# Performance work log

Measured on AMD Instinct MI355X. Metric: run time of the kernel, lower is better.

The kernel has to match this reference:

```python
import jax, jax.numpy as jnp
import numpy as np

B, T, I, H = 64, 512, 256, 1024


def setup_inputs() -> dict:
    key = jax.random.key(0)
    ks = jax.random.split(key, 20)
    stdv = float(1.0 / np.sqrt(H))
    u = lambda k, shape: jax.random.uniform(k, shape, jnp.float32, -stdv, stdv)
    d = {
        "inputs": jax.random.normal(ks[0], (B, T, I), jnp.float32),
        "h0": jax.random.normal(ks[1], (1, B, H), jnp.float32),
        "c0": jax.random.normal(ks[2], (1, B, H), jnp.float32),
    }
    names = ["w_ii", "w_hi", "b_ii", "b_hi",
             "w_if", "w_hf", "b_if", "b_hf",
             "w_io", "w_ho", "b_io", "b_ho",
             "w_ig", "w_hg", "b_ig", "b_hg"]
    shapes = {"w_i": (H, I), "w_h": (H, H), "b_i": (H,), "b_h": (H,)}
    for j, n in enumerate(names):
        d[n] = u(ks[3 + j], shapes[n[:3]])
    return d


def reference(inputs, h0, c0,
              w_ii, w_hi, b_ii, b_hi,
              w_if, w_hf, b_if, b_hf,
              w_io, w_ho, b_io, b_ho,
              w_ig, w_hg, b_ig, b_hg):
    # Fuse the 4 gate GEMMs into one: gate order i, f, g, o.
    Wx = jnp.concatenate([w_ii, w_if, w_ig, w_io], axis=0)  # (4H, I)
    Wh = jnp.concatenate([w_hi, w_hf, w_hg, w_ho], axis=0)  # (4H, H)
    b = jnp.concatenate([b_ii + b_hi, b_if + b_hf, b_ig + b_hg, b_io + b_ho], axis=0)  # (4H,)
    # Precompute all input projections in one big GEMM: (T, B, 4H)
    x_proj = jnp.einsum('bti,gi->tbg', inputs, Wx) + b

    def step(carry, xp):
        h, c = carry                       # (B, H), (B, H)
        z = xp + h @ Wh.T                  # (B, 4H)
        i = jax.nn.sigmoid(z[:, :H])
        f = jax.nn.sigmoid(z[:, H:2 * H])
        g = jnp.tanh(z[:, 2 * H:3 * H])
        o = jax.nn.sigmoid(z[:, 3 * H:])
        c = f * c + i * g
        h = o * jnp.tanh(c)
        return (h, c), h

    (h, c), hs = jax.lax.scan(step, (h0[0], c0[0]), x_proj)
    hidden_seq = jnp.transpose(hs, (1, 0, 2))  # (B, T, H)
    return hidden_seq, (h[None], c[None])
```

## Files before the change

kernel.cpp:

```cpp
#include <hip/hip_runtime.h>
#include <hip/hip_bf16.h>

#define TT 512
#define BB 64
#define II 256
#define HH 1024
#define NWG 256
#define MB 16
#define NJ 16
#define NR 64
#define KTOT 1280
#define WU 120
#define WROWB 1920
#define HROWB 2048
#define NFLAG 1024

typedef __bf16 bf16x8 __attribute__((ext_vector_type(8)));
typedef float f32x4 __attribute__((ext_vector_type(4)));
typedef unsigned uint32x4 __attribute__((ext_vector_type(4)));
typedef unsigned uint32x2 __attribute__((ext_vector_type(2)));

__device__ inline uint32x4 ld16_sc1(const void* p) {
  uint32x4 r;
  asm volatile("global_load_dwordx4 %0, %1, off sc1" : "=&v"(r) : "v"(p));
  return r;
}


__global__ __launch_bounds__(256) void k_cast_inputs(const float* __restrict__ in,
                                                     __hip_bfloat16* __restrict__ outp) {
  int i = (blockIdx.x * 256 + threadIdx.x) * 4;
  float4 v = *reinterpret_cast<const float4*>(in + i);
  outp[i + 0] = __float2bfloat16(v.x);
  outp[i + 1] = __float2bfloat16(v.y);
  outp[i + 2] = __float2bfloat16(v.z);
  outp[i + 3] = __float2bfloat16(v.w);
}

__global__ __launch_bounds__(256) void k_pack_w(
    const float* __restrict__ wxi, const float* __restrict__ whi,
    const float* __restrict__ wxf, const float* __restrict__ whf,
    const float* __restrict__ wxg, const float* __restrict__ whg,
    const float* __restrict__ wxo, const float* __restrict__ who,
    __hip_bfloat16* __restrict__ Wp) {
  int t = blockIdx.x * 256 + threadIdx.x;
  int p = t / 320;
  int k4 = (t - p * 320) * 4;
  int j = p >> 2, gate = p & 3;
  const float* wx = (gate == 0) ? wxi : (gate == 1) ? wxf : (gate == 2) ? wxg : wxo;
  const float* wh = (gate == 0) ? whi : (gate == 1) ? whf : (gate == 2) ? whg : who;
  float4 v;
  if (k4 < II) v = *reinterpret_cast<const float4*>(wx + (size_t)j * II + k4);
  else         v = *reinterpret_cast<const float4*>(wh + (size_t)j * HH + (k4 - II));
  __hip_bfloat16* o = Wp + (size_t)p * KTOT + k4;
  o[0] = __float2bfloat16(v.x);
  o[1] = __float2bfloat16(v.y);
  o[2] = __float2bfloat16(v.z);
  o[3] = __float2bfloat16(v.w);
}

__global__ __launch_bounds__(256) void k_pack_bias_h0(
    const float* __restrict__ bii, const float* __restrict__ bhi,
    const float* __restrict__ bif, const float* __restrict__ bhf,
    const float* __restrict__ bg,  const float* __restrict__ bhg,
    const float* __restrict__ bio, const float* __restrict__ bho,
    const float* __restrict__ h0, float* __restrict__ biasp,
    __hip_bfloat16* __restrict__ hb, unsigned* __restrict__ flags) {
  int i = blockIdx.x * 256 + threadIdx.x;
  if (i < 4096) {
    int j = i >> 2, gate = i & 3;
    const float* bi = (gate == 0) ? bii : (gate == 1) ? bif : (gate == 2) ? bg : bio;
    const float* bh = (gate == 0) ? bhi : (gate == 1) ? bhf : (gate == 2) ? bhg : bho;
    biasp[i] = bi[j] + bh[j];
  }
  if (i < NFLAG) flags[i] = 0;
  hb[i] = __float2bfloat16(h0[i]);
}


__global__ __launch_bounds__(256, 1) void k_lstm(
    const __hip_bfloat16* __restrict__ xb,
    const __hip_bfloat16* __restrict__ Wp,
    const float* __restrict__ biasp,
    const float* __restrict__ c0,
    __hip_bfloat16* __restrict__ hbuf,
    unsigned* __restrict__ flags,
    float* __restrict__ out)
{
  extern __shared__ __align__(16) char smem[];
  char* Wl = smem;
  char* Hs = smem + 122880;
  char* Zx = smem + 155648;
  char* Ho = smem + 160768;

  const int tid = threadIdx.x;
  const int lane = tid & 63;
  const int wq = tid >> 6;
  const int bt = blockIdx.x >> 6;
  const int gt = blockIdx.x & 63;
  const int b0 = bt * MB;
  const int r0 = gt * NR;

  const int l15 = lane & 15;
  const int kqu = lane >> 4;

  {
    const int u = tid & 127;
    const bool act = u < WU;
    uint32x4 tmp[16];
#pragma unroll
    for (int q = 0; q < 16; ++q) {
      int row = q * 2 + (tid >> 7);
      if (act) tmp[q] = *reinterpret_cast<const uint32x4*>(
          Wp + (size_t)(r0 + row) * KTOT + II + u * 8);
    }
#pragma unroll
    for (int q = 0; q < 16; ++q) {
      int row = q * 2 + (tid >> 7);
      if (act) *reinterpret_cast<uint32x4*>(Wl + row * WROWB + ((u ^ (row & 7)) << 4)) = tmp[q];
    }
#pragma unroll
    for (int q = 0; q < 16; ++q) {
      int row = 32 + q * 2 + (tid >> 7);
      if (act) tmp[q] = *reinterpret_cast<const uint32x4*>(
          Wp + (size_t)(r0 + row) * KTOT + II + u * 8);
    }
#pragma unroll
    for (int q = 0; q < 16; ++q) {
      int row = 32 + q * 2 + (tid >> 7);
      if (act) *reinterpret_cast<uint32x4*>(Wl + row * WROWB + ((u ^ (row & 7)) << 4)) = tmp[q];
    }
  }

  const int brow = r0 + wq * 16 + l15;
  bf16x8 wxr[8], wht0, wht1;
  {
    const __hip_bfloat16* ws = Wp + (size_t)brow * KTOT + kqu * 8;
#pragma unroll
    for (int kk = 0; kk < 8; ++kk)
      wxr[kk] = *reinterpret_cast<const bf16x8*>(ws + kk * 32);
    wht0 = *reinterpret_cast<const bf16x8*>(ws + II + 960);
    wht1 = *reinterpret_cast<const bf16x8*>(ws + II + 992);
  }

  const int m_e = 4 * kqu + (lane & 3);
  const int tq = (lane >> 2) & 3;
  const int j_g = gt * NJ + wq * 4 + tq;
  const int b_g = b0 + m_e;
  const float4 bias = *reinterpret_cast<const float4*>(biasp + j_g * 4);
  float c_reg = c0[(size_t)b_g * HH + j_g];

  const int hs_swz = l15 & 7;
  const int bn_row = wq * 16 + l15;
  const int bn_swz = bn_row & 7;
  char* ZxW = Zx + wq * 1280;
  char* HoW = Ho + wq * 128;

  {
    uint32x4 tmp[8];
#pragma unroll
    for (int q = 0; q < 8; ++q) {
      int idx = q * 64 + lane;
      int rl = wq * 4 + (idx >> 7);
      int u = idx & 127;
      tmp[q] = ld16_sc1(hbuf + (size_t)(b0 + rl) * HH + u * 8);
    }
    asm volatile("s_waitcnt vmcnt(0)" ::: "memory");
    __builtin_amdgcn_sched_barrier(0);
#pragma unroll
    for (int q = 0; q < 8; ++q) {
      int idx = q * 64 + lane;
      int rl = wq * 4 + (idx >> 7);
      int u = idx & 127;
      *reinterpret_cast<uint32x4*>(Hs + rl * HROWB + ((u ^ (rl & 7)) << 4)) = tmp[q];
    }
  }

  const __hip_bfloat16* xrowA = xb + (size_t)(b0 + l15) * (TT * II) + kqu * 8;
  f32x4 accs[4];
#pragma unroll
  for (int q = 0; q < 4; ++q) accs[q] = (f32x4){0.f, 0.f, 0.f, 0.f};
#pragma unroll
  for (int kk = 0; kk < 8; ++kk) {
    bf16x8 xa = *reinterpret_cast<const bf16x8*>(xrowA + kk * 32);
    accs[kk & 3] = __builtin_amdgcn_mfma_f32_16x16x32_bf16(xa, wxr[kk], accs[kk & 3], 0, 0, 0);
  }

  __syncthreads();

  for (int t = 0; t < TT; ++t) {
#pragma unroll
    for (int kk = 0; kk < 30; ++kk) {
      int u = kk * 4 + kqu;
      bf16x8 a = *reinterpret_cast<const bf16x8*>(Hs + l15 * HROWB + ((u ^ hs_swz) << 4));
      bf16x8 b = *reinterpret_cast<const bf16x8*>(Wl + bn_row * WROWB + ((u ^ bn_swz) << 4));
      accs[kk & 3] = __builtin_amdgcn_mfma_f32_16x16x32_bf16(a, b, accs[kk & 3], 0, 0, 0);
    }
    {
      int u = 120 + kqu;
      bf16x8 a = *reinterpret_cast<const bf16x8*>(Hs + l15 * HROWB + ((u ^ hs_swz) << 4));
      accs[2] = __builtin_amdgcn_mfma_f32_16x16x32_bf16(a, wht0, accs[2], 0, 0, 0);
    }
    {
      int u = 124 + kqu;
      bf16x8 a = *reinterpret_cast<const bf16x8*>(Hs + l15 * HROWB + ((u ^ hs_swz) << 4));
      accs[3] = __builtin_amdgcn_mfma_f32_16x16x32_bf16(a, wht1, accs[3], 0, 0, 0);
    }
    f32x4 acc = (accs[0] + accs[1]) + (accs[2] + accs[3]);

    *reinterpret_cast<f32x4*>(ZxW + l15 * 80 + kqu * 16) = acc;
    asm volatile("s_waitcnt lgkmcnt(0)" ::: "memory");
    __builtin_amdgcn_sched_barrier(0);
    float zi = *reinterpret_cast<const float*>(ZxW + (4 * tq + 0) * 80 + m_e * 4) + bias.x;
    float zf = *reinterpret_cast<const float*>(ZxW + (4 * tq + 1) * 80 + m_e * 4) + bias.y;
    float zg = *reinterpret_cast<const float*>(ZxW + (4 * tq + 2) * 80 + m_e * 4) + bias.z;
    float zo = *reinterpret_cast<const float*>(ZxW + (4 * tq + 3) * 80 + m_e * 4) + bias.w;

    float ig = 1.f / (1.f + __expf(-zi));
    float fg = 1.f / (1.f + __expf(-zf));
    float gg = 2.f / (1.f + __expf(-2.f * zg)) - 1.f;
    float og = 1.f / (1.f + __expf(-zo));
    c_reg = fg * c_reg + ig * gg;
    float tc = 2.f / (1.f + __expf(-2.f * c_reg)) - 1.f;
    float h = og * tc;

    if (t == TT - 1) {
      out[(size_t)b_g * (TT * HH) + (size_t)t * HH + j_g] = h;
      out[(size_t)BB * TT * HH + (size_t)b_g * HH + j_g] = h;
      out[(size_t)BB * TT * HH + BB * HH + (size_t)b_g * HH + j_g] = c_reg;
      break;
    }

    __hip_bfloat16 hb16 = __float2bfloat16(h);
    *reinterpret_cast<unsigned short*>(HoW + m_e * 8 + tq * 2) =
        *reinterpret_cast<unsigned short*>(&hb16);
    asm volatile("s_waitcnt lgkmcnt(0)" ::: "memory");
    __builtin_amdgcn_sched_barrier(0);

    const int nxt = (t + 1) & 1;
    if (lane < 16) {
      uint32x2 hv = *reinterpret_cast<const uint32x2*>(HoW + lane * 8);
      __hip_bfloat16* dst = hbuf + (size_t)nxt * (BB * HH)
                          + (size_t)(b0 + lane) * HH + gt * NJ + wq * 4;
      asm volatile("global_store_dwordx2 %0, %1, off sc1" :: "v"(dst), "v"(hv) : "memory");
    }
    asm volatile("s_waitcnt vmcnt(0)" ::: "memory");
    if (lane == 0) {
      unsigned gen = (unsigned)t + 1u;
      asm volatile("global_store_dword %0, %1, off sc1"
                   :: "v"(flags + bt * 256 + gt * 4 + wq), "v"(gen) : "memory");
    }

    out[(size_t)b_g * (TT * HH) + (size_t)t * HH + j_g] = h;
#pragma unroll
    for (int q = 0; q < 4; ++q) accs[q] = (f32x4){0.f, 0.f, 0.f, 0.f};
    {
      const __hip_bfloat16* xp = xrowA + (size_t)(t + 1) * II;
#pragma unroll
      for (int kk = 0; kk < 8; ++kk) {
        bf16x8 xa = *reinterpret_cast<const bf16x8*>(xp + kk * 32);
        accs[kk & 3] = __builtin_amdgcn_mfma_f32_16x16x32_bf16(xa, wxr[kk], accs[kk & 3], 0, 0, 0);
      }
    }

    {
      const unsigned target = (unsigned)t + 1u;
      const unsigned* fp = flags + bt * 256 + lane * 4;
      uint32x4 f;
      int ok;
      do {
        asm volatile("global_load_dwordx4 %0, %1, off sc1\n\ts_waitcnt vmcnt(0)"
                     : "=&v"(f) : "v"(fp) : "memory");
        ok = (f.x >= target) && (f.y >= target) && (f.z >= target) && (f.w >= target);
      } while (!__all(ok));
    }

    {
      uint32x4 tmp[8];
      const __hip_bfloat16* hsrc = hbuf + (size_t)nxt * (BB * HH);
#pragma unroll
      for (int q = 0; q < 8; ++q) {
        int idx = q * 64 + lane;
        int rl = wq * 4 + (idx >> 7);
        int u = idx & 127;
        tmp[q] = ld16_sc1(hsrc + (size_t)(b0 + rl) * HH + u * 8);
      }
      asm volatile("s_waitcnt vmcnt(0)" ::: "memory");
      __builtin_amdgcn_sched_barrier(0);
#pragma unroll
      for (int q = 0; q < 8; ++q) {
        int idx = q * 64 + lane;
        int rl = wq * 4 + (idx >> 7);
        int u = idx & 127;
        *reinterpret_cast<uint32x4*>(Hs + rl * HROWB + ((u ^ (rl & 7)) << 4)) = tmp[q];
      }
    }
    __syncthreads();
  }
}


extern "C" void kernel_launch(void* const* d_in, const int* in_sizes, int n_in,
                              void* d_out, int out_size, void* d_ws, size_t ws_size,
                              hipStream_t stream) {
  (void)in_sizes; (void)n_in; (void)out_size; (void)ws_size;
  const float* inputs = (const float*)d_in[0];
  const float* h0 = (const float*)d_in[1];
  const float* c0 = (const float*)d_in[2];
  const float* w_ii = (const float*)d_in[3];
  const float* w_hi = (const float*)d_in[4];
  const float* b_ii = (const float*)d_in[5];
  const float* b_hi = (const float*)d_in[6];
  const float* w_if = (const float*)d_in[7];
  const float* w_hf = (const float*)d_in[8];
  const float* b_if = (const float*)d_in[9];
  const float* b_hf = (const float*)d_in[10];
  const float* w_io = (const float*)d_in[11];
  const float* w_ho = (const float*)d_in[12];
  const float* b_io = (const float*)d_in[13];
  const float* b_ho = (const float*)d_in[14];
  const float* w_ig = (const float*)d_in[15];
  const float* w_hg = (const float*)d_in[16];
  const float* b_ig = (const float*)d_in[17];
  const float* b_hg = (const float*)d_in[18];

  char* ws = (char*)d_ws;
  __hip_bfloat16* xb    = (__hip_bfloat16*)ws;
  __hip_bfloat16* Wp    = (__hip_bfloat16*)(ws + 16777216);
  float*          biasp = (float*)(ws + 27262976);
  __hip_bfloat16* hbuf  = (__hip_bfloat16*)(ws + 27279360);
  unsigned*       flags = (unsigned*)(ws + 27541504);
  float* out = (float*)d_out;

  k_cast_inputs<<<8192, 256, 0, stream>>>(inputs, xb);
  k_pack_w<<<5120, 256, 0, stream>>>(w_ii, w_hi, w_if, w_hf, w_ig, w_hg, w_io, w_ho, Wp);
  k_pack_bias_h0<<<256, 256, 0, stream>>>(b_ii, b_hi, b_if, b_hf, b_ig, b_hg,
                                          b_io, b_ho, h0, biasp, hbuf, flags);

  const int lds_bytes = 161280;
  hipFuncSetAttribute((const void*)k_lstm,
                      hipFuncAttributeMaxDynamicSharedMemorySize, lds_bytes);
  void* args[] = {(void*)&xb, (void*)&Wp, (void*)&biasp, (void*)&c0,
                  (void*)&hbuf, (void*)&flags, (void*)&out};
  hipLaunchCooperativeKernel((void*)k_lstm, dim3(NWG), dim3(256), args,
                             lds_bytes, stream);
}
```

Measured before the change: 2.181 ms.

## Replace flag-based step barrier with generation-tagged hidden-state words

Each hidden value is now published as a 32-bit word that packs a step-generation tag in the high half with the bf16 value in the low half. Consumers poll the hidden-state data directly until every tag matches. This removes the separate flag stores, the store-then-flag ordering wait, and the LDS staging of outputs. The cost is twice the bytes per hidden-state exchange, scattered 4-byte stores, and retry reloads of the whole 32 KB slice when any value is stale.

```diff
diff --git a/kernel.cpp b/kernel.cpp
--- a/kernel.cpp
+++ b/kernel.cpp
@@ -13,7 +13,8 @@
 #define WU 120
 #define WROWB 1920
 #define HROWB 2048
-#define NFLAG 1024
+#define HW32 65536
+#define MAXTRY (1 << 20)
 
 typedef __bf16 bf16x8 __attribute__((ext_vector_type(8)));
 typedef float f32x4 __attribute__((ext_vector_type(4)));
@@ -24,6 +25,17 @@
   uint32x4 r;
   asm volatile("global_load_dwordx4 %0, %1, off sc1" : "=&v"(r) : "v"(p));
   return r;
+}
+
+__device__ inline void stage_issue(uint32x4 (&tmp)[16], const unsigned* __restrict__ hsrc,
+                                   int b0, int wq, int lane) {
+#pragma unroll
+  for (int q = 0; q < 16; ++q) {
+    int idx = q * 64 + lane;
+    int rl = wq * 4 + (idx >> 8);
+    int uq = idx & 255;
+    tmp[q] = ld16_sc1(hsrc + (size_t)(b0 + rl) * HH + uq * 4);
+  }
 }
 
 
@@ -65,7 +77,7 @@
     const float* __restrict__ bg,  const float* __restrict__ bhg,
     const float* __restrict__ bio, const float* __restrict__ bho,
     const float* __restrict__ h0, float* __restrict__ biasp,
-    __hip_bfloat16* __restrict__ hb, unsigned* __restrict__ flags) {
+    unsigned* __restrict__ hb) {
   int i = blockIdx.x * 256 + threadIdx.x;
   if (i < 4096) {
     int j = i >> 2, gate = i & 3;
@@ -73,8 +85,9 @@
     const float* bh = (gate == 0) ? bhi : (gate == 1) ? bhf : (gate == 2) ? bhg : bho;
     biasp[i] = bi[j] + bh[j];
   }
-  if (i < NFLAG) flags[i] = 0;
-  hb[i] = __float2bfloat16(h0[i]);
+  __hip_bfloat16 v = __float2bfloat16(h0[i]);
+  hb[i] = (unsigned)*reinterpret_cast<unsigned short*>(&v);
+  hb[HW32 + i] = 0u;
 }
 
 
@@ -83,15 +96,13 @@
     const __hip_bfloat16* __restrict__ Wp,
     const float* __restrict__ biasp,
     const float* __restrict__ c0,
-    __hip_bfloat16* __restrict__ hbuf,
-    unsigned* __restrict__ flags,
+    unsigned* __restrict__ hbuf,
     float* __restrict__ out)
 {
   extern __shared__ __align__(16) char smem[];
   char* Wl = smem;
   char* Hs = smem + 122880;
   char* Zx = smem + 155648;
-  char* Ho = smem + 160768;
 
   const int tid = threadIdx.x;
   const int lane = tid & 63;
@@ -107,28 +118,28 @@
   {
     const int u = tid & 127;
     const bool act = u < WU;
-    uint32x4 tmp[16];
+    uint32x4 wtmp[16];
 #pragma unroll
     for (int q = 0; q < 16; ++q) {
       int row = q * 2 + (tid >> 7);
-      if (act) tmp[q] = *reinterpret_cast<const uint32x4*>(
+      if (act) wtmp[q] = *reinterpret_cast<const uint32x4*>(
           Wp + (size_t)(r0 + row) * KTOT + II + u * 8);
     }
 #pragma unroll
     for (int q = 0; q < 16; ++q) {
       int row = q * 2 + (tid >> 7);
-      if (act) *reinterpret_cast<uint32x4*>(Wl + row * WROWB + ((u ^ (row & 7)) << 4)) = tmp[q];
+      if (act) *reinterpret_cast<uint32x4*>(Wl + row * WROWB + ((u ^ (row & 7)) << 4)) = wtmp[q];
     }
 #pragma unroll
     for (int q = 0; q < 16; ++q) {
       int row = 32 + q * 2 + (tid >> 7);
-      if (act) tmp[q] = *reinterpret_cast<const uint32x4*>(
+      if (act) wtmp[q] = *reinterpret_cast<const uint32x4*>(
           Wp + (size_t)(r0 + row) * KTOT + II + u * 8);
     }
 #pragma unroll
     for (int q = 0; q < 16; ++q) {
       int row = 32 + q * 2 + (tid >> 7);
-      if (act) *reinterpret_cast<uint32x4*>(Wl + row * WROWB + ((u ^ (row & 7)) << 4)) = tmp[q];
+      if (act) *reinterpret_cast<uint32x4*>(Wl + row * WROWB + ((u ^ (row & 7)) << 4)) = wtmp[q];
     }
   }
 
@@ -154,26 +165,34 @@
   const int bn_row = wq * 16 + l15;
   const int bn_swz = bn_row & 7;
   char* ZxW = Zx + wq * 1280;
-  char* HoW = Ho + wq * 128;
-
+
+  uint32x4 tmp[16];
+
+  stage_issue(tmp, hbuf, b0, wq, lane);
   {
-    uint32x4 tmp[8];
-#pragma unroll
-    for (int q = 0; q < 8; ++q) {
-      int idx = q * 64 + lane;
-      int rl = wq * 4 + (idx >> 7);
-      int u = idx & 127;
-      tmp[q] = ld16_sc1(hbuf + (size_t)(b0 + rl) * HH + u * 8);
-    }
-    asm volatile("s_waitcnt vmcnt(0)" ::: "memory");
-    __builtin_amdgcn_sched_barrier(0);
-#pragma unroll
-    for (int q = 0; q < 8; ++q) {
-      int idx = q * 64 + lane;
-      int rl = wq * 4 + (idx >> 7);
-      int u = idx & 127;
-      *reinterpret_cast<uint32x4*>(Hs + rl * HROWB + ((u ^ (rl & 7)) << 4)) = tmp[q];
-    }
+    int tries = 0;
+    for (;;) {
+      asm volatile("s_waitcnt vmcnt(0)" ::: "memory");
+      __builtin_amdgcn_sched_barrier(0);
+      unsigned bad = 0;
+#pragma unroll
+      for (int q = 0; q < 16; ++q) {
+        bad |= (tmp[q].x >> 16); bad |= (tmp[q].y >> 16);
+        bad |= (tmp[q].z >> 16); bad |= (tmp[q].w >> 16);
+      }
+      if (__all(bad == 0) || ++tries > MAXTRY) break;
+      stage_issue(tmp, hbuf, b0, wq, lane);
+    }
+  }
+#pragma unroll
+  for (int q = 0; q < 16; ++q) {
+    int idx = q * 64 + lane;
+    int rl = wq * 4 + (idx >> 8);
+    int uq = idx & 255;
+    unsigned lo = (tmp[q].x & 0xFFFFu) | (tmp[q].y << 16);
+    unsigned hi = (tmp[q].z & 0xFFFFu) | (tmp[q].w << 16);
+    *reinterpret_cast<uint32x2*>(Hs + rl * HROWB + ((((uq >> 1) ^ (rl & 7)) << 4) + (uq & 1) * 8))
+        = (uint32x2){lo, hi};
   }
 
   const __hip_bfloat16* xrowA = xb + (size_t)(b0 + l15) * (TT * II) + kqu * 8;
@@ -231,24 +250,13 @@
       break;
     }
 
-    __hip_bfloat16 hb16 = __float2bfloat16(h);
-    *reinterpret_cast<unsigned short*>(HoW + m_e * 8 + tq * 2) =
-        *reinterpret_cast<unsigned short*>(&hb16);
-    asm volatile("s_waitcnt lgkmcnt(0)" ::: "memory");
-    __builtin_amdgcn_sched_barrier(0);
-
     const int nxt = (t + 1) & 1;
-    if (lane < 16) {
-      uint32x2 hv = *reinterpret_cast<const uint32x2*>(HoW + lane * 8);
-      __hip_bfloat16* dst = hbuf + (size_t)nxt * (BB * HH)
-                          + (size_t)(b0 + lane) * HH + gt * NJ + wq * 4;
-      asm volatile("global_store_dwordx2 %0, %1, off sc1" :: "v"(dst), "v"(hv) : "memory");
-    }
-    asm volatile("s_waitcnt vmcnt(0)" ::: "memory");
-    if (lane == 0) {
-      unsigned gen = (unsigned)t + 1u;
-      asm volatile("global_store_dword %0, %1, off sc1"
-                   :: "v"(flags + bt * 256 + gt * 4 + wq), "v"(gen) : "memory");
+    const unsigned gen = (unsigned)(t + 1);
+    {
+      __hip_bfloat16 hb16 = __float2bfloat16(h);
+      unsigned pub = (gen << 16) | (unsigned)*reinterpret_cast<unsigned short*>(&hb16);
+      unsigned* dst = hbuf + (size_t)nxt * HW32 + (size_t)b_g * HH + j_g;
+      asm volatile("global_store_dword %0, %1, off sc1" :: "v"(dst), "v"(pub) : "memory");
     }
 
     out[(size_t)b_g * (TT * HH) + (size_t)t * HH + j_g] = h;
@@ -262,38 +270,35 @@
         accs[kk & 3] = __builtin_amdgcn_mfma_f32_16x16x32_bf16(xa, wxr[kk], accs[kk & 3], 0, 0, 0);
       }
     }
-
-    {
-      const unsigned target = (unsigned)t + 1u;
-      const unsigned* fp = flags + bt * 256 + lane * 4;
-      uint32x4 f;
-      int ok;
-      do {
-        asm volatile("global_load_dwordx4 %0, %1, off sc1\n\ts_waitcnt vmcnt(0)"
-                     : "=&v"(f) : "v"(fp) : "memory");
-        ok = (f.x >= target) && (f.y >= target) && (f.z >= target) && (f.w >= target);
-      } while (!__all(ok));
-    }
-
-    {
-      uint32x4 tmp[8];
-      const __hip_bfloat16* hsrc = hbuf + (size_t)nxt * (BB * HH);
-#pragma unroll
-      for (int q = 0; q < 8; ++q) {
-        int idx = q * 64 + lane;
-        int rl = wq * 4 + (idx >> 7);
-        int u = idx & 127;
-        tmp[q] = ld16_sc1(hsrc + (size_t)(b0 + rl) * HH + u * 8);
+    const unsigned* hsrc = hbuf + (size_t)nxt * HW32;
+    stage_issue(tmp, hsrc, b0, wq, lane);
+
+    __syncthreads();
+
+    {
+      int tries = 0;
+      for (;;) {
+        asm volatile("s_waitcnt vmcnt(0)" ::: "memory");
+        __builtin_amdgcn_sched_barrier(0);
+        unsigned bad = 0;
+#pragma unroll
+        for (int q = 0; q < 16; ++q) {
+          bad |= (tmp[q].x >> 16) ^ gen; bad |= (tmp[q].y >> 16) ^ gen;
+          bad |= (tmp[q].z >> 16) ^ gen; bad |= (tmp[q].w >> 16) ^ gen;
+        }
+        if (__all(bad == 0) || ++tries > MAXTRY) break;
+        stage_issue(tmp, hsrc, b0, wq, lane);
       }
-      asm volatile("s_waitcnt vmcnt(0)" ::: "memory");
-      __builtin_amdgcn_sched_barrier(0);
-#pragma unroll
-      for (int q = 0; q < 8; ++q) {
-        int idx = q * 64 + lane;
-        int rl = wq * 4 + (idx >> 7);
-        int u = idx & 127;
-        *reinterpret_cast<uint32x4*>(Hs + rl * HROWB + ((u ^ (rl & 7)) << 4)) = tmp[q];
-      }
+    }
+#pragma unroll
+    for (int q = 0; q < 16; ++q) {
+      int idx = q * 64 + lane;
+      int rl = wq * 4 + (idx >> 8);
+      int uq = idx & 255;
+      unsigned lo = (tmp[q].x & 0xFFFFu) | (tmp[q].y << 16);
+      unsigned hi = (tmp[q].z & 0xFFFFu) | (tmp[q].w << 16);
+      *reinterpret_cast<uint32x2*>(Hs + rl * HROWB + ((((uq >> 1) ^ (rl & 7)) << 4) + (uq & 1) * 8))
+          = (uint32x2){lo, hi};
     }
     __syncthreads();
   }
@@ -328,20 +333,22 @@
   __hip_bfloat16* xb    = (__hip_bfloat16*)ws;
   __hip_bfloat16* Wp    = (__hip_bfloat16*)(ws + 16777216);
   float*          biasp = (float*)(ws + 27262976);
-  __hip_bfloat16* hbuf  = (__hip_bfloat16*)(ws + 27279360);
-  unsigned*       flags = (unsigned*)(ws + 27541504);
+  unsigned*       hbuf  = (unsigned*)(ws + 27279360);
   float* out = (float*)d_out;
 
   k_cast_inputs<<<8192, 256, 0, stream>>>(inputs, xb);
   k_pack_w<<<5120, 256, 0, stream>>>(w_ii, w_hi, w_if, w_hf, w_ig, w_hg, w_io, w_ho, Wp);
   k_pack_bias_h0<<<256, 256, 0, stream>>>(b_ii, b_hi, b_if, b_hf, b_ig, b_hg,
-                                          b_io, b_ho, h0, biasp, hbuf, flags);
-
-  const int lds_bytes = 161280;
+                                          b_io, b_ho, h0, biasp, hbuf);
+
+  const int lds_bytes = 160768;
   hipFuncSetAttribute((const void*)k_lstm,
                       hipFuncAttributeMaxDynamicSharedMemorySize, lds_bytes);
   void* args[] = {(void*)&xb, (void*)&Wp, (void*)&biasp, (void*)&c0,
-                  (void*)&hbuf, (void*)&flags, (void*)&out};
-  hipLaunchCooperativeKernel((void*)k_lstm, dim3(NWG), dim3(256), args,
-                             lds_bytes, stream);
-}
+                  (void*)&hbuf, (void*)&out};
+  hipError_t e = hipLaunchCooperativeKernel((void*)k_lstm, dim3(NWG), dim3(256),
+                                            args, lds_bytes, stream);
+  if (e != hipSuccess) {
+    k_lstm<<<dim3(NWG), dim3(256), lds_bytes, stream>>>(xb, Wp, biasp, c0, hbuf, out);
+  }
+}
```

New measurement: 2.446 ms. 1.12x slower.

## Use per-workgroup padded flags with single-wave polling and block barriers

Applied to the files above, without the earlier changes.

Replaces the per-wave generation flags with one flag per workgroup, padded to 64 bytes, published by thread 0 after a block barrier. Only wave 0 polls the 64 flags of its batch tile, one dword per lane, and the other waves wait at a __syncthreads. This cuts flag-polling traffic and contention on shared cache lines, at the cost of two extra block barriers per timestep. It also adds a bounded spin count and a plain-launch fallback if the cooperative launch fails.

```diff
diff --git a/kernel.cpp b/kernel.cpp
--- a/kernel.cpp
+++ b/kernel.cpp
@@ -13,7 +13,8 @@
 #define WU 120
 #define WROWB 1920
 #define HROWB 2048
-#define NFLAG 1024
+#define FPAD 16
+#define MAXTRY (1 << 20)
 
 typedef __bf16 bf16x8 __attribute__((ext_vector_type(8)));
 typedef float f32x4 __attribute__((ext_vector_type(4)));
@@ -72,8 +73,8 @@
     const float* bi = (gate == 0) ? bii : (gate == 1) ? bif : (gate == 2) ? bg : bio;
     const float* bh = (gate == 0) ? bhi : (gate == 1) ? bhf : (gate == 2) ? bhg : bho;
     biasp[i] = bi[j] + bh[j];
-  }
-  if (i < NFLAG) flags[i] = 0;
+    flags[i] = 0;
+  }
   hb[i] = __float2bfloat16(h0[i]);
 }
 
@@ -107,28 +108,28 @@
   {
     const int u = tid & 127;
     const bool act = u < WU;
-    uint32x4 tmp[16];
+    uint32x4 wtmp[16];
 #pragma unroll
     for (int q = 0; q < 16; ++q) {
       int row = q * 2 + (tid >> 7);
-      if (act) tmp[q] = *reinterpret_cast<const uint32x4*>(
+      if (act) wtmp[q] = *reinterpret_cast<const uint32x4*>(
           Wp + (size_t)(r0 + row) * KTOT + II + u * 8);
     }
 #pragma unroll
     for (int q = 0; q < 16; ++q) {
       int row = q * 2 + (tid >> 7);
-      if (act) *reinterpret_cast<uint32x4*>(Wl + row * WROWB + ((u ^ (row & 7)) << 4)) = tmp[q];
+      if (act) *reinterpret_cast<uint32x4*>(Wl + row * WROWB + ((u ^ (row & 7)) << 4)) = wtmp[q];
     }
 #pragma unroll
     for (int q = 0; q < 16; ++q) {
       int row = 32 + q * 2 + (tid >> 7);
-      if (act) tmp[q] = *reinterpret_cast<const uint32x4*>(
+      if (act) wtmp[q] = *reinterpret_cast<const uint32x4*>(
           Wp + (size_t)(r0 + row) * KTOT + II + u * 8);
     }
 #pragma unroll
     for (int q = 0; q < 16; ++q) {
       int row = 32 + q * 2 + (tid >> 7);
-      if (act) *reinterpret_cast<uint32x4*>(Wl + row * WROWB + ((u ^ (row & 7)) << 4)) = tmp[q];
+      if (act) *reinterpret_cast<uint32x4*>(Wl + row * WROWB + ((u ^ (row & 7)) << 4)) = wtmp[q];
     }
   }
 
@@ -238,6 +239,7 @@
     __builtin_amdgcn_sched_barrier(0);
 
     const int nxt = (t + 1) & 1;
+    const unsigned gen = (unsigned)(t + 1);
     if (lane < 16) {
       uint32x2 hv = *reinterpret_cast<const uint32x2*>(HoW + lane * 8);
       __hip_bfloat16* dst = hbuf + (size_t)nxt * (BB * HH)
@@ -245,10 +247,12 @@
       asm volatile("global_store_dwordx2 %0, %1, off sc1" :: "v"(dst), "v"(hv) : "memory");
     }
     asm volatile("s_waitcnt vmcnt(0)" ::: "memory");
-    if (lane == 0) {
-      unsigned gen = (unsigned)t + 1u;
+
+    __syncthreads();
+
+    if (tid == 0) {
       asm volatile("global_store_dword %0, %1, off sc1"
-                   :: "v"(flags + bt * 256 + gt * 4 + wq), "v"(gen) : "memory");
+                   :: "v"(flags + (bt * 64 + gt) * FPAD), "v"(gen) : "memory");
     }
 
     out[(size_t)b_g * (TT * HH) + (size_t)t * HH + j_g] = h;
@@ -263,17 +267,17 @@
       }
     }
 
-    {
-      const unsigned target = (unsigned)t + 1u;
-      const unsigned* fp = flags + bt * 256 + lane * 4;
-      uint32x4 f;
-      int ok;
-      do {
-        asm volatile("global_load_dwordx4 %0, %1, off sc1\n\ts_waitcnt vmcnt(0)"
+    if (wq == 0) {
+      const unsigned* fp = flags + (bt * 64 + lane) * FPAD;
+      int tries = 0;
+      unsigned f;
+      for (;;) {
+        asm volatile("global_load_dword %0, %1, off sc1\n\ts_waitcnt vmcnt(0)"
                      : "=&v"(f) : "v"(fp) : "memory");
-        ok = (f.x >= target) && (f.y >= target) && (f.z >= target) && (f.w >= target);
-      } while (!__all(ok));
-    }
+        if (__all(f >= gen) || ++tries > MAXTRY) break;
+      }
+    }
+    __syncthreads();
 
     {
       uint32x4 tmp[8];
@@ -342,6 +346,9 @@
                       hipFuncAttributeMaxDynamicSharedMemorySize, lds_bytes);
   void* args[] = {(void*)&xb, (void*)&Wp, (void*)&biasp, (void*)&c0,
                   (void*)&hbuf, (void*)&flags, (void*)&out};
-  hipLaunchCooperativeKernel((void*)k_lstm, dim3(NWG), dim3(256), args,
-                             lds_bytes, stream);
-}
+  hipError_t e = hipLaunchCooperativeKernel((void*)k_lstm, dim3(NWG), dim3(256),
+                                            args, lds_bytes, stream);
+  if (e != hipSuccess) {
+    k_lstm<<<dim3(NWG), dim3(256), lds_bytes, stream>>>(xb, Wp, biasp, c0, hbuf, flags, out);
+  }
+}
```

New measurement: 2.281 ms. 4.6% more time.

## Keep recurrent weight slice in registers instead of LDS

Applied to the files above, without the earlier changes.

Each lane now preloads all 32 of its recurrent-weight fragments (bf16x8) into registers once. The per-step MFMA loop therefore reads only the hidden state from LDS, and LDS use drops from about 160KB to 38KB (131072 requested). This removes per-step LDS traffic and bank pressure for the weight operand, at the cost of a large increase in VGPR use (about 128 more registers), which could cause spilling. The change also adds a bounded spin-wait on the flags and a fallback to a normal launch if the cooperative launch fails.

```diff
diff --git a/kernel.cpp b/kernel.cpp
--- a/kernel.cpp
+++ b/kernel.cpp
@@ -10,10 +10,9 @@
 #define NJ 16
 #define NR 64
 #define KTOT 1280
-#define WU 120
-#define WROWB 1920
 #define HROWB 2048
 #define NFLAG 1024
+#define MAXTRY (1 << 20)
 
 typedef __bf16 bf16x8 __attribute__((ext_vector_type(8)));
 typedef float f32x4 __attribute__((ext_vector_type(4)));
@@ -88,10 +87,9 @@
     float* __restrict__ out)
 {
   extern __shared__ __align__(16) char smem[];
-  char* Wl = smem;
-  char* Hs = smem + 122880;
-  char* Zx = smem + 155648;
-  char* Ho = smem + 160768;
+  char* Hs = smem;
+  char* Zx = smem + 32768;
+  char* Ho = smem + 37888;
 
   const int tid = threadIdx.x;
   const int lane = tid & 63;
@@ -104,43 +102,17 @@
   const int l15 = lane & 15;
   const int kqu = lane >> 4;
 
-  {
-    const int u = tid & 127;
-    const bool act = u < WU;
-    uint32x4 tmp[16];
-#pragma unroll
-    for (int q = 0; q < 16; ++q) {
-      int row = q * 2 + (tid >> 7);
-      if (act) tmp[q] = *reinterpret_cast<const uint32x4*>(
-          Wp + (size_t)(r0 + row) * KTOT + II + u * 8);
-    }
-#pragma unroll
-    for (int q = 0; q < 16; ++q) {
-      int row = q * 2 + (tid >> 7);
-      if (act) *reinterpret_cast<uint32x4*>(Wl + row * WROWB + ((u ^ (row & 7)) << 4)) = tmp[q];
-    }
-#pragma unroll
-    for (int q = 0; q < 16; ++q) {
-      int row = 32 + q * 2 + (tid >> 7);
-      if (act) tmp[q] = *reinterpret_cast<const uint32x4*>(
-          Wp + (size_t)(r0 + row) * KTOT + II + u * 8);
-    }
-#pragma unroll
-    for (int q = 0; q < 16; ++q) {
-      int row = 32 + q * 2 + (tid >> 7);
-      if (act) *reinterpret_cast<uint32x4*>(Wl + row * WROWB + ((u ^ (row & 7)) << 4)) = tmp[q];
-    }
-  }
-
   const int brow = r0 + wq * 16 + l15;
-  bf16x8 wxr[8], wht0, wht1;
+  bf16x8 wxr[8], whr[32];
   {
     const __hip_bfloat16* ws = Wp + (size_t)brow * KTOT + kqu * 8;
 #pragma unroll
     for (int kk = 0; kk < 8; ++kk)
       wxr[kk] = *reinterpret_cast<const bf16x8*>(ws + kk * 32);
-    wht0 = *reinterpret_cast<const bf16x8*>(ws + II + 960);
-    wht1 = *reinterpret_cast<const bf16x8*>(ws + II + 992);
+    const __hip_bfloat16* wh = ws + II;
+#pragma unroll
+    for (int kk = 0; kk < 32; ++kk)
+      whr[kk] = *reinterpret_cast<const bf16x8*>(wh + kk * 32);
   }
 
   const int m_e = 4 * kqu + (lane & 3);
@@ -151,8 +123,6 @@
   float c_reg = c0[(size_t)b_g * HH + j_g];
 
   const int hs_swz = l15 & 7;
-  const int bn_row = wq * 16 + l15;
-  const int bn_swz = bn_row & 7;
   char* ZxW = Zx + wq * 1280;
   char* HoW = Ho + wq * 128;
 
@@ -190,21 +160,10 @@
 
   for (int t = 0; t < TT; ++t) {
 #pragma unroll
-    for (int kk = 0; kk < 30; ++kk) {
+    for (int kk = 0; kk < 32; ++kk) {
       int u = kk * 4 + kqu;
       bf16x8 a = *reinterpret_cast<const bf16x8*>(Hs + l15 * HROWB + ((u ^ hs_swz) << 4));
-      bf16x8 b = *reinterpret_cast<const bf16x8*>(Wl + bn_row * WROWB + ((u ^ bn_swz) << 4));
-      accs[kk & 3] = __builtin_amdgcn_mfma_f32_16x16x32_bf16(a, b, accs[kk & 3], 0, 0, 0);
-    }
-    {
-      int u = 120 + kqu;
-      bf16x8 a = *reinterpret_cast<const bf16x8*>(Hs + l15 * HROWB + ((u ^ hs_swz) << 4));
-      accs[2] = __builtin_amdgcn_mfma_f32_16x16x32_bf16(a, wht0, accs[2], 0, 0, 0);
-    }
-    {
-      int u = 124 + kqu;
-      bf16x8 a = *reinterpret_cast<const bf16x8*>(Hs + l15 * HROWB + ((u ^ hs_swz) << 4));
-      accs[3] = __builtin_amdgcn_mfma_f32_16x16x32_bf16(a, wht1, accs[3], 0, 0, 0);
+      accs[kk & 3] = __builtin_amdgcn_mfma_f32_16x16x32_bf16(a, whr[kk], accs[kk & 3], 0, 0, 0);
     }
     f32x4 acc = (accs[0] + accs[1]) + (accs[2] + accs[3]);
 
@@ -238,6 +197,7 @@
     __builtin_amdgcn_sched_barrier(0);
 
     const int nxt = (t + 1) & 1;
+    const unsigned gen = (unsigned)(t + 1);
     if (lane < 16) {
       uint32x2 hv = *reinterpret_cast<const uint32x2*>(HoW + lane * 8);
       __hip_bfloat16* dst = hbuf + (size_t)nxt * (BB * HH)
@@ -246,7 +206,6 @@
     }
     asm volatile("s_waitcnt vmcnt(0)" ::: "memory");
     if (lane == 0) {
-      unsigned gen = (unsigned)t + 1u;
       asm volatile("global_store_dword %0, %1, off sc1"
                    :: "v"(flags + bt * 256 + gt * 4 + wq), "v"(gen) : "memory");
     }
@@ -264,15 +223,15 @@
     }
 
     {
-      const unsigned target = (unsigned)t + 1u;
       const unsigned* fp = flags + bt * 256 + lane * 4;
+      int tries = 0;
       uint32x4 f;
-      int ok;
-      do {
+      for (;;) {
         asm volatile("global_load_dwordx4 %0, %1, off sc1\n\ts_waitcnt vmcnt(0)"
                      : "=&v"(f) : "v"(fp) : "memory");
-        ok = (f.x >= target) && (f.y >= target) && (f.z >= target) && (f.w >= target);
-      } while (!__all(ok));
+        int ok = (f.x >= gen) && (f.y >= gen) && (f.z >= gen) && (f.w >= gen);
+        if (__all(ok) || ++tries > MAXTRY) break;
+      }
     }
 
     {
@@ -337,11 +296,14 @@
   k_pack_bias_h0<<<256, 256, 0, stream>>>(b_ii, b_hi, b_if, b_hf, b_ig, b_hg,
                                           b_io, b_ho, h0, biasp, hbuf, flags);
 
-  const int lds_bytes = 161280;
+  const int lds_bytes = 131072;
   hipFuncSetAttribute((const void*)k_lstm,
                       hipFuncAttributeMaxDynamicSharedMemorySize, lds_bytes);
   void* args[] = {(void*)&xb, (void*)&Wp, (void*)&biasp, (void*)&c0,
                   (void*)&hbuf, (void*)&flags, (void*)&out};
-  hipLaunchCooperativeKernel((void*)k_lstm, dim3(NWG), dim3(256), args,
-                             lds_bytes, stream);
-}
+  hipError_t e = hipLaunchCooperativeKernel((void*)k_lstm, dim3(NWG), dim3(256),
+                                            args, lds_bytes, stream);
+  if (e != hipSuccess) {
+    k_lstm<<<dim3(NWG), dim3(256), lds_bytes, stream>>>(xb, Wp, biasp, c0, hbuf, flags, out);
+  }
+}
```

New measurement: 1.904 ms. 12.7% less time.
